# Performance work log

Measured on AMD Instinct MI355X. Metric: run time of the kernel, lower is better.

## Reference

```python
import jax, jax.numpy as jnp
import numpy as np

TOPK = 13
NUM_CLASSES = 80
ALPHA = 1.0
BETA = 6.0
EPS = 1e-9
IMG = 640.0


def setup_inputs() -> dict:
    key = jax.random.key(0)
    k = jax.random.split(key, 8)
    bs, A, C, n = 32, 8400, NUM_CLASSES, 64
    pd_scores = jax.random.uniform(k[0], (bs, A, C), dtype=jnp.float32)
    # valid x1y1x2y2 predicted boxes
    ctr = jax.random.uniform(k[1], (bs, A, 2), dtype=jnp.float32) * IMG
    wh = jax.random.uniform(k[2], (bs, A, 2), dtype=jnp.float32) * 90.0 + 10.0
    pd_bboxes = jnp.concatenate([ctr - wh / 2, ctr + wh / 2], axis=-1)
    anc_points = jax.random.uniform(k[3], (8400, 2), dtype=jnp.float32) * IMG
    gt_labels = jax.random.randint(k[4], (bs, n, 1), 0, C, dtype=jnp.int64)
    gctr = jax.random.uniform(k[5], (bs, n, 2), dtype=jnp.float32) * IMG
    gwh = jax.random.uniform(k[6], (bs, n, 2), dtype=jnp.float32) * 140.0 + 20.0
    gt_bboxes = jnp.concatenate([gctr - gwh / 2, gctr + gwh / 2], axis=-1)
    mask_gt = (jax.random.uniform(k[7], (bs, n, 1)) < 0.8).astype(jnp.float32)
    return {"pd_scores": pd_scores, "pd_bboxes": pd_bboxes, "anc_points": anc_points,
            "gt_labels": gt_labels, "gt_bboxes": gt_bboxes, "mask_gt": mask_gt}


def _assign(pd_scores, pd_bboxes, anc_points, gt_labels, gt_bboxes, mask_gt):
    b, A, C = pd_scores.shape
    n = gt_bboxes.shape[1]
    gl = gt_labels.reshape(b, n).astype(jnp.int32)

    # bbox_scores[b,n,a] = pd_scores[b, a, gt_labels[b,n]]  -> (b, n, A)
    bbox_scores = jnp.take_along_axis(pd_scores.transpose(0, 2, 1), gl[:, :, None], axis=1)

    # pairwise IoU: gt (b,n,1,4) vs pred (b,1,A,4) -> (b,n,A)
    b1 = gt_bboxes[:, :, None, :]
    b2 = pd_bboxes[:, None, :, :]
    lt = jnp.maximum(b1[..., :2], b2[..., :2])
    rb = jnp.minimum(b1[..., 2:], b2[..., 2:])
    overlap = jnp.clip(rb - lt, 0).prod(-1)
    area1 = jnp.clip(b1[..., 2:] - b1[..., :2], 0).prod(-1)
    area2 = jnp.clip(b2[..., 2:] - b2[..., :2], 0).prod(-1)
    overlaps = overlap / (area1 + area2 - overlap + EPS)

    align_metric = (bbox_scores ** ALPHA) * (overlaps ** BETA)

    # anchor centers inside gt boxes -> (b,n,A)
    lt_d = anc_points[None, None, :, :] - gt_bboxes[:, :, None, :2]
    rb_d = gt_bboxes[:, :, None, 2:] - anc_points[None, None, :, :]
    deltas = jnp.concatenate([lt_d, rb_d], axis=-1)
    mask_in_gts = (deltas.min(-1) > EPS).astype(gt_bboxes.dtype)

    # topk candidate selection with scatter-count (avoids (b,n,topk,A) one-hot)
    metrics = align_metric * mask_in_gts
    _, topk_idxs = jax.lax.top_k(metrics, TOPK)  # (b,n,TOPK)
    topk_mask = mask_gt.reshape(b, n, 1) != 0
    topk_idxs = jnp.where(topk_mask, topk_idxs, 0)
    bi = jnp.arange(b)[:, None, None]
    ni = jnp.arange(n)[None, :, None]
    counts = jnp.zeros((b, n, A), jnp.int32).at[bi, ni, topk_idxs].add(1)
    is_in_topk = jnp.where(counts > 1, 0, counts).astype(metrics.dtype)

    mask_pos = is_in_topk * mask_in_gts * mask_gt.reshape(b, n, 1)

    # resolve anchors assigned to multiple gts by highest IoU
    fg_mask = mask_pos.sum(-2)                         # (b,A)
    mask_multi = fg_mask[:, None, :] > 1               # (b,1,A) broadcast over n
    max_idx = overlaps.argmax(axis=1)                  # (b,A)
    is_max = jax.nn.one_hot(max_idx, n, dtype=overlaps.dtype).transpose(0, 2, 1)  # (b,n,A)
    mask_pos = jnp.where(mask_multi, is_max, mask_pos)
    fg_mask = mask_pos.sum(-2)
    target_gt_idx = mask_pos.argmax(-2)                # (b,A)

    # gather targets
    target_labels = jnp.take_along_axis(gl, target_gt_idx, axis=1)            # (b,A)
    target_labels = jnp.maximum(target_labels, 0)
    target_bboxes = jnp.take_along_axis(gt_bboxes, target_gt_idx[:, :, None], axis=1)  # (b,A,4)
    target_scores = jax.nn.one_hot(target_labels, C, dtype=pd_scores.dtype)
    target_scores = jnp.where(fg_mask[:, :, None] > 0, target_scores, 0.0)

    # normalize scores by alignment metric
    align_metric = align_metric * mask_pos
    pos_align = align_metric.max(-1, keepdims=True)                  # (b,n,1)
    pos_overlaps = (overlaps * mask_pos).max(-1, keepdims=True)      # (b,n,1)
    norm = (align_metric * pos_overlaps / (pos_align + EPS)).max(-2)[:, :, None]  # (b,A,1)
    target_scores = target_scores * norm

    return target_labels, target_bboxes, target_scores, fg_mask > 0


def reference(pd_scores, pd_bboxes, anc_points, gt_labels, gt_bboxes, mask_gt):
    return _assign(pd_scores, pd_bboxes, anc_points, gt_labels, gt_bboxes, mask_gt)
```

## Files before the change

### kernel.cpp

```cpp
#include <hip/hip_runtime.h>
#include <math.h>

#define A_N   8400
#define BS    32
#define NGT   64
#define NC    80
#define TK    13
#define EPSF  1e-9f
#define CAP   1024
#define JG    16
#define NJG   4
#define NTILE 33
#define PCAP  64
#define NCAND (BS * NTILE * NJG)
#define NASSIGN (BS * NTILE)

typedef float nt4 __attribute__((ext_vector_type(4)));

#define OFF_LB 0
#define OFF_BB (BS * A_N)
#define OFF_SC (OFF_BB + BS * A_N * 4)
#define OFF_FG (OFF_SC + BS * A_N * NC)

#define WS_CNT   0
#define WS_MINJ  (WS_CNT  + BS * A_N * 4)
#define WS_POSA  (WS_MINJ + BS * A_N * 4)
#define WS_POSO  (WS_POSA + BS * NGT * 4)
#define WS_CNT2  (WS_POSO + BS * NGT * 4)
#define WS_FGBC  (WS_CNT2 + BS * NGT * 4)
#define WS_FGL   (WS_FGBC + 4352)
#define WS_CAND  (WS_FGL  + NASSIGN * 256 * 16)


__device__ __forceinline__ float iou_f(float g0, float g1, float g2, float g3,
                                       float p0, float p1, float p2, float p3) {
    float ltx = fmaxf(g0, p0), lty = fmaxf(g1, p1);
    float rbx = fminf(g2, p2), rby = fminf(g3, p3);
    float ov  = fmaxf(rbx - ltx, 0.f) * fmaxf(rby - lty, 0.f);
    float a1  = fmaxf(g2 - g0, 0.f) * fmaxf(g3 - g1, 0.f);
    float a2  = fmaxf(p2 - p0, 0.f) * fmaxf(p3 - p1, 0.f);
    return ov / (a1 + a2 - ov + EPSF);
}

__device__ __forceinline__ int get_gl(const int* g, int flag64, int i) {
    return flag64 ? g[2 * i] : g[i];
}

__device__ __forceinline__ int probe_flag64_wave0(const int* gl_raw, int tid) {
    int f64 = 0;
    if (tid < 64) {
        unsigned long long m = __ballot(gl_raw[2 * tid + 1] != 0);
        f64 = (m == 0ull);
    }
    return f64;
}

__device__ __forceinline__ unsigned long long shfl_xor_u64(unsigned long long x, int m) {
    int lo = __shfl_xor((int)(unsigned int)(x & 0xFFFFFFFFull), m, 64);
    int hi = __shfl_xor((int)(unsigned int)(x >> 32), m, 64);
    return ((unsigned long long)(unsigned int)hi << 32) | (unsigned int)lo;
}

__global__ __launch_bounds__(256) void k_zero(int* __restrict__ base) {
    int i = blockIdx.x * 256 + threadIdx.x;
    if (i < 3 * BS * NGT) base[i] = 0;
}

__global__ __launch_bounds__(256) void k_cand(
    const float* __restrict__ pd_scores, const float* __restrict__ pd_bboxes,
    const float* __restrict__ anc, const int* __restrict__ gl_raw,
    const float* __restrict__ gt_bboxes, const float* __restrict__ mask_gt,
    int* __restrict__ cnt2, unsigned long long* __restrict__ cand,
    int* __restrict__ cnt, int* __restrict__ minj, float* __restrict__ out) {
    __shared__ float4 sgt[JG];
    __shared__ int    slbl[JG];
    __shared__ int    smask[JG];
    __shared__ int    cnt_lds[JG];
    __shared__ int    base_lds[JG];
    __shared__ unsigned long long pool[JG][PCAP];

    int bid  = blockIdx.x;
    int b    = bid / (NTILE * NJG);
    int rem  = bid % (NTILE * NJG);
    int tile = rem / NJG;
    int jg   = rem % NJG;
    int tid  = threadIdx.x;
    int a    = tile * 256 + tid;
    int jbase = b * NGT + jg * JG;

    int f64 = probe_flag64_wave0(gl_raw, tid);
    if (tid < JG) {
        sgt[tid]   = ((const float4*)gt_bboxes)[jbase + tid];
        slbl[tid]  = get_gl(gl_raw, f64, jbase + tid);
        smask[tid] = (mask_gt[jbase + tid] != 0.f);
        cnt_lds[tid] = 0;
    }
    __syncthreads();

    bool act = (a < A_N);
    float2 an = make_float2(0.f, 0.f);
    float4 p  = make_float4(0.f, 0.f, 0.f, 0.f);
    const float* sc = pd_scores;
    if (act) {
        an = ((const float2*)anc)[a];
        p  = ((const float4*)pd_bboxes)[(size_t)b * A_N + a];
        sc = pd_scores + (size_t)b * A_N * NC + (size_t)a * NC;
    }

    for (int j = 0; j < JG; j++) {
        if (!smask[j]) continue;
        if (!act) continue;
        float4 g = sgt[j];
        float d = fminf(fminf(an.x - g.x, an.y - g.y),
                        fminf(g.z - an.x, g.w - an.y));
        if (d > EPSF) {
            float iou = iou_f(g.x, g.y, g.z, g.w, p.x, p.y, p.z, p.w);
            float m = 0.f;
            if (iou > 0.f) {
                float s = sc[slbl[j]];
                m = s * powf(iou, 6.0f);
            }
            unsigned long long key =
                ((unsigned long long)__float_as_uint(m) << 32) |
                (unsigned int)(~(unsigned int)a);
            int slot = atomicAdd(&cnt_lds[j], 1);
            if (slot < PCAP) {
                pool[j][slot] = key;
            } else {
                int gs = atomicAdd(&cnt2[jbase + j], 1);
                if (gs < CAP) cand[(size_t)(jbase + j) * CAP + gs] = key;
            }
        }
    }
    __syncthreads();

    if (tid < JG) {
        int c = min(cnt_lds[tid], PCAP);
        int bas = 0;
        if (c > 0) bas = atomicAdd(&cnt2[jbase + tid], c);
        base_lds[tid] = bas;
    }
    __syncthreads();

    for (int j = 0; j < JG; j++) {
        int c = min(cnt_lds[j], PCAP);
        int bas = base_lds[j];
        for (int t = tid; t < c; t += 256) {
            int dst = bas + t;
            if (dst < CAP) cand[(size_t)(jbase + j) * CAP + dst] = pool[j][t];
        }
    }

    {
        int gth = bid * 256 + tid;
        const int GS = NCAND * 256;
        nt4* scz = (nt4*)(out + OFF_SC);
        for (int t = gth; t < BS * A_N * (NC / 4); t += GS)
            __builtin_nontemporal_store((nt4)(0.f), &scz[t]);
        for (int t = gth; t < BS * A_N; t += GS) {
            cnt[t] = 0; minj[t] = 1 << 30;
        }
    }
}

template <int NT>
__device__ __forceinline__ void pick_body(
    int lane, int b, int j, int n, const unsigned long long* __restrict__ L,
    int* __restrict__ cnt, int* __restrict__ minj) {
    unsigned long long k0[NT];
    #pragma unroll
    for (int t = 0; t < NT; t++) {
        int i = t * 64 + lane;
        k0[t] = (i < n) ? L[i] : 0ULL;
    }

    unsigned int wanchor[TK];
    int P = 0;
    #pragma unroll
    for (int r = 0; r < TK; r++) {
        unsigned long long best = 0;
        #pragma unroll
        for (int t = 0; t < NT; t++) best = (k0[t] > best) ? k0[t] : best;
        for (int s = 1; s < 64; s <<= 1) {
            unsigned long long o = shfl_xor_u64(best, s);
            if (o > best) best = o;
        }
        if (!(best >> 32)) break;
        unsigned int aw = ~(unsigned int)(best & 0xFFFFFFFFull);
        wanchor[r] = aw;
        if (lane == 0) {
            atomicAdd(&cnt[b * A_N + (int)aw], 1);
            atomicMin(&minj[b * A_N + (int)aw], j);
        }
        #pragma unroll
        for (int t = 0; t < NT; t++) if (k0[t] == best) k0[t] = 0;
        P++;
    }

    if (P < TK) {
        int K = TK - P;
        #pragma unroll
        for (int t = 0; t < NT; t++) {
            unsigned long long key = k0[t];
            if (key != 0 && !(key >> 32)) {
                unsigned int a0 = ~(unsigned int)(key & 0xFFFFFFFFull);
                int off = 0;
                #pragma unroll
                for (int r = 0; r < TK; r++)
                    if (r < P && wanchor[r] < a0) off++;
                if ((int)a0 < K + off) {
                    atomicAdd(&cnt[b * A_N + (int)a0], 1);
                    atomicMin(&minj[b * A_N + (int)a0], j);
                }
            }
        }
    }
}

__global__ __launch_bounds__(256) void k_pick(
    const int* __restrict__ cnt2, const unsigned long long* __restrict__ cand,
    int* __restrict__ cnt, int* __restrict__ minj) {
    int lane = threadIdx.x & 63;
    int wave = threadIdx.x >> 6;
    int bj = blockIdx.x * 4 + wave;
    int b = bj >> 6, j = bj & 63;

    int n = min(cnt2[bj], CAP);
    if (n == 0) return;
    const unsigned long long* L = cand + (size_t)bj * CAP;

    if (n <= 128)      pick_body<2>(lane, b, j, n, L, cnt, minj);
    else if (n <= 320) pick_body<5>(lane, b, j, n, L, cnt, minj);
    else               pick_body<16>(lane, b, j, n, L, cnt, minj);
}

__global__ __launch_bounds__(256) void k_assign(
    const float* __restrict__ pd_scores, const float* __restrict__ pd_bboxes,
    const float* __restrict__ gt_bboxes, const int* __restrict__ gl_raw,
    const int* __restrict__ cnt, const int* __restrict__ minj,
    unsigned int* posA, unsigned int* posO,
    int4* __restrict__ fgList, int* __restrict__ fgBlockCnt,
    float* __restrict__ out) {
    __shared__ float4 sgb[NGT];
    __shared__ int    slb[NGT];
    __shared__ int    swc[4];

    int tid = threadIdx.x;
    int b   = blockIdx.x / NTILE;
    int a   = (blockIdx.x % NTILE) * 256 + tid;

    int f64 = probe_flag64_wave0(gl_raw, tid);
    if (tid < NGT) {
        sgb[tid] = ((const float4*)gt_bboxes)[b * NGT + tid];
        int l = get_gl(gl_raw, f64, b * NGT + tid);
        slb[tid] = (l < 0) ? 0 : l;
    }
    __syncthreads();

    bool act = (a < A_N);
    int i = b * A_N + a;

    int c = 0, mj = 0;
    float4 p = make_float4(0.f, 0.f, 0.f, 0.f);
    if (act) {
        c  = cnt[i];
        mj = minj[i];
        p  = ((const float4*)pd_bboxes)[i];
    }

    int jstar = 0;
    if (act) {
        if (c == 1) {
            jstar = mj;
        } else if (c > 1) {
            float bv = -1.f; int bj_ = 0;
            for (int j = 0; j < NGT; j++) {
                float4 g = sgb[j];
                float ov = iou_f(g.x, g.y, g.z, g.w, p.x, p.y, p.z, p.w);
                if (ov > bv) { bv = ov; bj_ = j; }
            }
            jstar = bj_;
        }
    }

    int fg = (act && c > 0) ? 1 : 0;
    float al = 0.f;
    int lbl = 0;
    if (act) {
        lbl = slb[jstar];
        out[OFF_LB + i] = (float)lbl;
        float4 g = sgb[jstar];
        ((float4*)(out + OFF_BB))[i] = g;
        out[OFF_FG + i] = (float)fg;
        if (fg) {
            float ov = iou_f(g.x, g.y, g.z, g.w, p.x, p.y, p.z, p.w);
            float s  = pd_scores[(size_t)i * NC + lbl];
            al = s * powf(ov, 6.0f);
            atomicMax((int*)&posA[b * NGT + jstar], __float_as_int(al));
            atomicMax((int*)&posO[b * NGT + jstar], __float_as_int(ov));
        }
    }

    int lane = tid & 63;
    int wv   = tid >> 6;
    unsigned long long mv = __ballot(fg != 0);
    if (lane == 0) swc[wv] = (int)__popcll(mv);
    __syncthreads();
    int w0 = swc[0], w1 = swc[1], w2 = swc[2], w3 = swc[3];
    if (fg) {
        int pre = (wv > 0 ? w0 : 0) + (wv > 1 ? w1 : 0) + (wv > 2 ? w2 : 0);
        int rank = pre + (int)__popcll(mv & ((1ull << lane) - 1ull));
        fgList[blockIdx.x * 256 + rank] =
            make_int4(i | (lbl << 20), b * NGT + jstar, __float_as_int(al), 0);
    }
    if (tid == 0) fgBlockCnt[blockIdx.x] = w0 + w1 + w2 + w3;
}

__global__ __launch_bounds__(256) void k_norm(
    const int4* __restrict__ fgList, const int* __restrict__ fgBlockCnt,
    const unsigned int* __restrict__ posA, const unsigned int* __restrict__ posO,
    float* __restrict__ out) {
    int bb = blockIdx.x;
    int t  = threadIdx.x;
    int n  = fgBlockCnt[bb];
    if (t >= n) return;
    int4 r  = fgList[bb * 256 + t];
    int i   = r.x & 0xFFFFF;
    int lbl = r.x >> 20;
    int bj  = r.y;
    float al = __int_as_float(r.z);
    float pa = __int_as_float((int)posA[bj]);
    float po = __int_as_float((int)posO[bj]);
    out[OFF_SC + (size_t)i * NC + lbl] = al * po / (pa + EPSF);
}

extern "C" void kernel_launch(void* const* d_in, const int* in_sizes, int n_in,
                              void* d_out, int out_size, void* d_ws, size_t ws_size,
                              hipStream_t stream) {
    const float* pd_scores = (const float*)d_in[0];
    const float* pd_bboxes = (const float*)d_in[1];
    const float* anc       = (const float*)d_in[2];
    const int*   gl_raw    = (const int*)d_in[3];
    const float* gt_bboxes = (const float*)d_in[4];
    const float* mask_gt   = (const float*)d_in[5];
    float* out = (float*)d_out;

    char* ws = (char*)d_ws;
    int*                cnt      = (int*)(ws + WS_CNT);
    int*                minj     = (int*)(ws + WS_MINJ);
    unsigned int*       posA     = (unsigned int*)(ws + WS_POSA);
    unsigned int*       posO     = (unsigned int*)(ws + WS_POSO);
    int*                cnt2     = (int*)(ws + WS_CNT2);
    int*                fgBC     = (int*)(ws + WS_FGBC);
    int4*               fgList   = (int4*)(ws + WS_FGL);
    unsigned long long* cand     = (unsigned long long*)(ws + WS_CAND);

    k_zero<<<24, 256, 0, stream>>>((int*)(ws + WS_POSA));
    k_cand<<<NCAND, 256, 0, stream>>>(pd_scores, pd_bboxes, anc, gl_raw,
                                      gt_bboxes, mask_gt, cnt2, cand,
                                      cnt, minj, out);
    k_pick<<<BS * NGT / 4, 256, 0, stream>>>(cnt2, cand, cnt, minj);
    k_assign<<<NASSIGN, 256, 0, stream>>>(pd_scores, pd_bboxes, gt_bboxes,
                                          gl_raw, cnt, minj,
                                          posA, posO, fgList, fgBC, out);
    k_norm<<<NASSIGN, 256, 0, stream>>>(fgList, fgBC, posA, posO, out);
}
```

Before: 210.6 us.

## Replace global per-anchor count/minj atomics with per-GT pick lists resolved in LDS

New measurement: 209.7 us. Within noise of the previous version (-0.4%).

```diff
diff --git a/kernel.cpp b/kernel.cpp
--- a/kernel.cpp
+++ b/kernel.cpp
@@ -14,6 +14,7 @@
 #define PCAP  64
 #define NCAND (BS * NTILE * NJG)
 #define NASSIGN (BS * NTILE)
+#define PKW   16
 
 typedef float nt4 __attribute__((ext_vector_type(4)));
 
@@ -22,13 +23,13 @@
 #define OFF_SC (OFF_BB + BS * A_N * 4)
 #define OFF_FG (OFF_SC + BS * A_N * NC)
 
-#define WS_CNT   0
-#define WS_MINJ  (WS_CNT  + BS * A_N * 4)
-#define WS_POSA  (WS_MINJ + BS * A_N * 4)
+#define WS_POSA  0
 #define WS_POSO  (WS_POSA + BS * NGT * 4)
 #define WS_CNT2  (WS_POSO + BS * NGT * 4)
-#define WS_FGBC  (WS_CNT2 + BS * NGT * 4)
-#define WS_FGL   (WS_FGBC + 4352)
+#define WS_PKC   (WS_CNT2 + BS * NGT * 4)
+#define WS_PKL   (WS_PKC  + BS * NGT * 4)
+#define WS_FGBC  (WS_PKL  + BS * NGT * PKW * 4)
+#define WS_FGL   (WS_FGBC + 8192)
 #define WS_CAND  (WS_FGL  + NASSIGN * 256 * 16)
 
 
@@ -61,9 +62,9 @@
     return ((unsigned long long)(unsigned int)hi << 32) | (unsigned int)lo;
 }
 
-__global__ __launch_bounds__(256) void k_zero(int* __restrict__ base) {
+__global__ __launch_bounds__(256) void k_zero(int* __restrict__ cnt2) {
     int i = blockIdx.x * 256 + threadIdx.x;
-    if (i < 3 * BS * NGT) base[i] = 0;
+    if (i < BS * NGT) cnt2[i] = 0;
 }
 
 __global__ __launch_bounds__(256) void k_cand(
@@ -71,7 +72,7 @@
     const float* __restrict__ anc, const int* __restrict__ gl_raw,
     const float* __restrict__ gt_bboxes, const float* __restrict__ mask_gt,
     int* __restrict__ cnt2, unsigned long long* __restrict__ cand,
-    int* __restrict__ cnt, int* __restrict__ minj, float* __restrict__ out) {
+    int* __restrict__ posZero, float* __restrict__ out) {
     __shared__ float4 sgt[JG];
     __shared__ int    slbl[JG];
     __shared__ int    smask[JG];
@@ -157,16 +158,14 @@
         nt4* scz = (nt4*)(out + OFF_SC);
         for (int t = gth; t < BS * A_N * (NC / 4); t += GS)
             __builtin_nontemporal_store((nt4)(0.f), &scz[t]);
-        for (int t = gth; t < BS * A_N; t += GS) {
-            cnt[t] = 0; minj[t] = 1 << 30;
-        }
+        if (gth < 2 * BS * NGT) posZero[gth] = 0;
     }
 }
 
 template <int NT>
 __device__ __forceinline__ void pick_body(
-    int lane, int b, int j, int n, const unsigned long long* __restrict__ L,
-    int* __restrict__ cnt, int* __restrict__ minj) {
+    int lane, int bj, int n, const unsigned long long* __restrict__ L,
+    int* __restrict__ pickList, int* __restrict__ pickCnt) {
     unsigned long long k0[NT];
     #pragma unroll
     for (int t = 0; t < NT; t++) {
@@ -186,69 +185,79 @@
             if (o > best) best = o;
         }
         if (!(best >> 32)) break;
-        unsigned int aw = ~(unsigned int)(best & 0xFFFFFFFFull);
-        wanchor[r] = aw;
-        if (lane == 0) {
-            atomicAdd(&cnt[b * A_N + (int)aw], 1);
-            atomicMin(&minj[b * A_N + (int)aw], j);
-        }
+        wanchor[r] = ~(unsigned int)(best & 0xFFFFFFFFull);
         #pragma unroll
         for (int t = 0; t < NT; t++) if (k0[t] == best) k0[t] = 0;
         P++;
     }
 
+    #pragma unroll
+    for (int r = 0; r < TK; r++)
+        if (r < P && lane == 0) pickList[bj * PKW + r] = (int)wanchor[r];
+
+    int base = P;
     if (P < TK) {
         int K = TK - P;
         #pragma unroll
         for (int t = 0; t < NT; t++) {
             unsigned long long key = k0[t];
-            if (key != 0 && !(key >> 32)) {
-                unsigned int a0 = ~(unsigned int)(key & 0xFFFFFFFFull);
-                int off = 0;
-                #pragma unroll
-                for (int r = 0; r < TK; r++)
-                    if (r < P && wanchor[r] < a0) off++;
-                if ((int)a0 < K + off) {
-                    atomicAdd(&cnt[b * A_N + (int)a0], 1);
-                    atomicMin(&minj[b * A_N + (int)a0], j);
-                }
-            }
-        }
-    }
+            bool isf = (key != 0ULL) && !(key >> 32);
+            unsigned int a0 = ~(unsigned int)(key & 0xFFFFFFFFull);
+            int off = 0;
+            #pragma unroll
+            for (int r = 0; r < TK; r++)
+                if (r < P && wanchor[r] < a0) off++;
+            bool emit = isf && ((int)a0 < K + off);
+            unsigned long long mv = __ballot(emit);
+            if (emit) {
+                int rank = (int)__popcll(mv & ((1ull << lane) - 1ull));
+                pickList[bj * PKW + base + rank] = (int)a0;
+            }
+            base += (int)__popcll(mv);
+        }
+    }
+    if (lane == 0) pickCnt[bj] = base;
 }
 
 __global__ __launch_bounds__(256) void k_pick(
     const int* __restrict__ cnt2, const unsigned long long* __restrict__ cand,
-    int* __restrict__ cnt, int* __restrict__ minj) {
+    int* __restrict__ pickList, int* __restrict__ pickCnt) {
     int lane = threadIdx.x & 63;
     int wave = threadIdx.x >> 6;
     int bj = blockIdx.x * 4 + wave;
-    int b = bj >> 6, j = bj & 63;
 
     int n = min(cnt2[bj], CAP);
-    if (n == 0) return;
+    if (n == 0) {
+        if (lane == 0) pickCnt[bj] = 0;
+        return;
+    }
     const unsigned long long* L = cand + (size_t)bj * CAP;
 
-    if (n <= 128)      pick_body<2>(lane, b, j, n, L, cnt, minj);
-    else if (n <= 320) pick_body<5>(lane, b, j, n, L, cnt, minj);
-    else               pick_body<16>(lane, b, j, n, L, cnt, minj);
+    if (n <= 128)      pick_body<2>(lane, bj, n, L, pickList, pickCnt);
+    else if (n <= 320) pick_body<5>(lane, bj, n, L, pickList, pickCnt);
+    else               pick_body<16>(lane, bj, n, L, pickList, pickCnt);
 }
 
 __global__ __launch_bounds__(256) void k_assign(
     const float* __restrict__ pd_scores, const float* __restrict__ pd_bboxes,
     const float* __restrict__ gt_bboxes, const int* __restrict__ gl_raw,
-    const int* __restrict__ cnt, const int* __restrict__ minj,
+    const int* __restrict__ pickList, const int* __restrict__ pickCnt,
     unsigned int* posA, unsigned int* posO,
     int4* __restrict__ fgList, int* __restrict__ fgBlockCnt,
     float* __restrict__ out) {
     __shared__ float4 sgb[NGT];
     __shared__ int    slb[NGT];
+    __shared__ int    scnt[256];
+    __shared__ int    smnj[256];
     __shared__ int    swc[4];
 
     int tid = threadIdx.x;
     int b   = blockIdx.x / NTILE;
-    int a   = (blockIdx.x % NTILE) * 256 + tid;
-
+    int lo  = (blockIdx.x % NTILE) * 256;
+    int a   = lo + tid;
+
+    scnt[tid] = 0;
+    smnj[tid] = 1 << 30;
     int f64 = probe_flag64_wave0(gl_raw, tid);
     if (tid < NGT) {
         sgb[tid] = ((const float4*)gt_bboxes)[b * NGT + tid];
@@ -257,16 +266,26 @@
     }
     __syncthreads();
 
+    if (tid < NGT) {
+        int j  = tid;
+        int pc = pickCnt[b * NGT + j];
+        for (int s = 0; s < pc; s++) {
+            int rel = pickList[(b * NGT + j) * PKW + s] - lo;
+            if ((unsigned)rel < 256u) {
+                atomicAdd(&scnt[rel], 1);
+                atomicMin(&smnj[rel], j);
+            }
+        }
+    }
+    __syncthreads();
+
     bool act = (a < A_N);
     int i = b * A_N + a;
 
-    int c = 0, mj = 0;
+    int c  = act ? scnt[tid] : 0;
+    int mj = smnj[tid];
     float4 p = make_float4(0.f, 0.f, 0.f, 0.f);
-    if (act) {
-        c  = cnt[i];
-        mj = minj[i];
-        p  = ((const float4*)pd_bboxes)[i];
-    }
+    if (act) p = ((const float4*)pd_bboxes)[i];
 
     int jstar = 0;
     if (act) {
@@ -288,10 +307,11 @@
     int lbl = 0;
     if (act) {
         lbl = slb[jstar];
-        out[OFF_LB + i] = (float)lbl;
+        __builtin_nontemporal_store((float)lbl, &out[OFF_LB + i]);
         float4 g = sgb[jstar];
-        ((float4*)(out + OFF_BB))[i] = g;
-        out[OFF_FG + i] = (float)fg;
+        nt4 gv; gv.x = g.x; gv.y = g.y; gv.z = g.z; gv.w = g.w;
+        __builtin_nontemporal_store(gv, &((nt4*)(out + OFF_BB))[i]);
+        __builtin_nontemporal_store((float)fg, &out[OFF_FG + i]);
         if (fg) {
             float ov = iou_f(g.x, g.y, g.z, g.w, p.x, p.y, p.z, p.w);
             float s  = pd_scores[(size_t)i * NC + lbl];
@@ -346,22 +366,22 @@
     float* out = (float*)d_out;
 
     char* ws = (char*)d_ws;
-    int*                cnt      = (int*)(ws + WS_CNT);
-    int*                minj     = (int*)(ws + WS_MINJ);
     unsigned int*       posA     = (unsigned int*)(ws + WS_POSA);
     unsigned int*       posO     = (unsigned int*)(ws + WS_POSO);
     int*                cnt2     = (int*)(ws + WS_CNT2);
+    int*                pickCnt  = (int*)(ws + WS_PKC);
+    int*                pickList = (int*)(ws + WS_PKL);
     int*                fgBC     = (int*)(ws + WS_FGBC);
     int4*               fgList   = (int4*)(ws + WS_FGL);
     unsigned long long* cand     = (unsigned long long*)(ws + WS_CAND);
 
-    k_zero<<<24, 256, 0, stream>>>((int*)(ws + WS_POSA));
+    k_zero<<<8, 256, 0, stream>>>(cnt2);
     k_cand<<<NCAND, 256, 0, stream>>>(pd_scores, pd_bboxes, anc, gl_raw,
                                       gt_bboxes, mask_gt, cnt2, cand,
-                                      cnt, minj, out);
-    k_pick<<<BS * NGT / 4, 256, 0, stream>>>(cnt2, cand, cnt, minj);
+                                      (int*)(ws + WS_POSA), out);
+    k_pick<<<BS * NGT / 4, 256, 0, stream>>>(cnt2, cand, pickList, pickCnt);
     k_assign<<<NASSIGN, 256, 0, stream>>>(pd_scores, pd_bboxes, gt_bboxes,
-                                          gl_raw, cnt, minj,
+                                          gl_raw, pickList, pickCnt,
                                           posA, posO, fgList, fgBC, out);
     k_norm<<<NASSIGN, 256, 0, stream>>>(fgList, fgBC, posA, posO, out);
 }
```
